# Performance work log

Hardware: AMD Instinct MI355X
Metric: run time of the kernel (lower is better)

Reference implementation:

```python
import jax, jax.numpy as jnp
import numpy as np

B, N, F, T, K, FO = 16, 1024, 64, 24, 3, 64


def setup_inputs() -> dict:
    key = jax.random.key(0)
    ks = jax.random.split(key, 8)
    sc = 0.05
    x = jax.random.normal(ks[0], (B, N, F, T), dtype=jnp.float32)
    W1 = jax.random.normal(ks[1], (T,), dtype=jnp.float32) * sc
    W2 = jax.random.normal(ks[2], (F, T), dtype=jnp.float32) * sc
    W3 = jax.random.normal(ks[3], (F,), dtype=jnp.float32) * sc
    bs = jax.random.normal(ks[4], (1, N, N), dtype=jnp.float32) * sc
    Vs = jax.random.normal(ks[5], (N, N), dtype=jnp.float32) * sc
    cheb = jax.random.normal(ks[6], (K, N, N), dtype=jnp.float32) * sc
    Theta = jax.random.normal(ks[7], (K, F, FO), dtype=jnp.float32) * sc
    return {"x": x, "W1": W1, "W2": W2, "W3": W3, "bs": bs, "Vs": Vs,
            "cheb": cheb, "Theta": Theta}


def spatial_attention(x, W1, W2, W3, bs, Vs):
    # x: (B,N,F,T) -> S: (B,N,N)
    lhs = jnp.einsum('bnft,t->bnf', x, W1)          # (B,N,F)
    lhs = jnp.einsum('bnf,ft->bnt', lhs, W2)        # (B,N,T)
    rhs = jnp.einsum('f,bnft->btn', W3, x)          # (B,T,N)
    product = jnp.einsum('bnt,btm->bnm', lhs, rhs)  # (B,N,N)
    S = jnp.einsum('ik,bkj->bij', Vs, jax.nn.sigmoid(product + bs))
    return jax.nn.softmax(S, axis=1)


def reference(x, W1, W2, W3, bs, Vs, cheb, Theta):
    # x: (B,N,F,T); cheb: (K,N,N); Theta: (K,F,FO)
    S = spatial_attention(x, W1, W2, W3, bs, Vs)    # (B,N,N)
    out = jnp.zeros((x.shape[0], x.shape[1], Theta.shape[2], x.shape[3]),
                    dtype=x.dtype)
    for k in range(cheb.shape[0]):                  # small fixed K
        Tat = cheb[k] * S                           # (B,N,N) attention-masked T_k
        # T_k_with_at.permute(0,2,1) @ graph_signal, vectorized over t
        r = jnp.einsum('bnm,bnft->bmft', Tat, x)    # (B,N,F,T)
        out = out + jnp.einsum('bmft,fo->bmot', r, Theta[k])
    return jax.nn.relu(out)                         # (B,N,FO,T)
```

## Files before the change

### kernel.cpp

```cpp
#include <hip/hip_runtime.h>
#include <math.h>

#define Bc 16
#define Nc 1024
#define Fc 64
#define Tc 24
#define Kc 3
#define FOc 64
#define Cc (Fc*Tc)
#define KKc (Kc*Nc)

typedef __attribute__((ext_vector_type(8))) short short8;
typedef __attribute__((ext_vector_type(8))) unsigned short u16x8;
typedef __attribute__((ext_vector_type(4))) float f32x4;

__device__ __forceinline__ unsigned short f2bf(float f) {
  unsigned u = __float_as_uint(f);
  u += 0x7fff + ((u >> 16) & 1);
  return (unsigned short)(u >> 16);
}
__device__ __forceinline__ float bf2f(unsigned short h) {
  return __uint_as_float((unsigned)h << 16);
}

#define GLL16(g, l) __builtin_amdgcn_global_load_lds( \
    (const __attribute__((address_space(1))) void*)(g), \
    (__attribute__((address_space(3))) void*)(l), 16, 0, 0)

__device__ __forceinline__ f32x4 mfma16(short8 a, short8 b, f32x4 c) {
  return __builtin_amdgcn_mfma_f32_16x16x32_bf16(a, b, c, 0, 0, 0);
}

__device__ __forceinline__ void gemm_core(
    const unsigned short* __restrict__ Ag, const unsigned short* __restrict__ Bg,
    int lda, int ldb, int K,
    unsigned short* As, unsigned short* Bs,
    int wave, int lane, f32x4 acc[4][4]) {
  int sr = lane >> 3;
  int sc = ((lane & 7) ^ sr) * 8;
  const unsigned short* a0 = Ag + (size_t)(wave * 32 + sr) * lda + sc;
  const unsigned short* b0 = Bg + (size_t)(wave * 32 + sr) * ldb + sc;
  unsigned short* asw = As + (wave * 32) * 64;
  unsigned short* bsw = Bs + (wave * 32) * 64;
  int rw = (wave >> 1) * 64, cw = (wave & 1) * 64;
  int frow = lane & 15;
  int q = lane >> 4;
  int p0 = (q ^ (frow & 7)) * 8;
  int p1 = ((q | 4) ^ (frow & 7)) * 8;
  for (int k0 = 0; k0 < K; k0 += 64) {
    #pragma unroll
    for (int c = 0; c < 4; ++c) {
      GLL16(a0 + (size_t)(c * 8) * lda + k0, asw + (c * 8) * 64);
      GLL16(b0 + (size_t)(c * 8) * ldb + k0, bsw + (c * 8) * 64);
    }
    __syncthreads();
    #pragma unroll
    for (int h = 0; h < 2; ++h) {
      int p = h ? p1 : p0;
      short8 afr[4], bfr[4];
      #pragma unroll
      for (int i = 0; i < 4; ++i)
        afr[i] = *(const short8*)&As[(rw + i * 16 + frow) * 64 + p];
      #pragma unroll
      for (int j = 0; j < 4; ++j)
        bfr[j] = *(const short8*)&Bs[(cw + j * 16 + frow) * 64 + p];
      #pragma unroll
      for (int i = 0; i < 4; ++i)
        #pragma unroll
        for (int j = 0; j < 4; ++j)
          acc[i][j] = mfma16(afr[i], bfr[j], acc[i][j]);
    }
    __syncthreads();
  }
}

__global__ __launch_bounds__(256) void xprep_kernel(
    const float* __restrict__ x, const float* __restrict__ W1,
    const float* __restrict__ W2, const float* __restrict__ W3,
    unsigned short* __restrict__ xt2, float* __restrict__ lhs,
    float* __restrict__ rhs) {
  __shared__ float ld[4 * 1560];
  __shared__ float af[4 * 64];
  int w = threadIdx.x >> 6, lane = threadIdx.x & 63;
  size_t n = (size_t)blockIdx.x * 4 + w;
  const float* xp = x + n * Cc;
  float* lw = ld + w * 1560;
  #pragma unroll
  for (int j = 0; j < 24; ++j) {
    int i = j * 64 + lane;
    int f = i / 24, t = i - f * 24;
    lw[t * 65 + f] = xp[i];
  }
  __syncthreads();
  float a = 0.f;
  #pragma unroll
  for (int t = 0; t < Tc; ++t) a += lw[t * 65 + lane] * W1[t];
  af[w * 64 + lane] = a;
  #pragma unroll
  for (int j = 0; j < 24; ++j)
    xt2[n * Cc + j * 64 + lane] = f2bf(lw[j * 65 + lane]);
  __syncthreads();
  if (lane < Tc) {
    float l = 0.f, r = 0.f;
    #pragma unroll 8
    for (int f = 0; f < Fc; ++f) {
      l += af[w * 64 + f] * W2[f * Tc + lane];
      r += W3[f] * lw[lane * 65 + f];
    }
    lhs[n * Tc + lane] = l;
    rhs[n * Tc + lane] = r;
  }
}

__global__ __launch_bounds__(256) void prodsigT_kernel(
    const float* __restrict__ lhs, const float* __restrict__ rhs,
    const float* __restrict__ bs, unsigned short* __restrict__ sigT) {
  int b = blockIdx.z;
  int p0 = blockIdx.y * 64, q0 = blockIdx.x * 64;
  __shared__ float Ls[64 * 25], Rs[64 * 25], Bt[64 * 65];
  int tid = threadIdx.x;
  const float* lp = lhs + ((size_t)b * Nc + q0) * Tc;
  const float* rp = rhs + ((size_t)b * Nc + p0) * Tc;
  for (int i = tid; i < 64 * Tc; i += 256) {
    Ls[(i / Tc) * 25 + i % Tc] = lp[i];
    Rs[(i / Tc) * 25 + i % Tc] = rp[i];
  }
  for (int i = tid; i < 1024; i += 256) {
    int qr = i >> 4, pc = (i & 15) * 4;
    *(float4*)&Bt[qr * 65 + pc] = *(const float4*)&bs[(size_t)(q0 + qr) * Nc + p0 + pc];
  }
  __syncthreads();
  int tx = tid % 16, ty = tid / 16;
  float acc[4][4] = {};
  for (int t = 0; t < Tc; ++t) {
    float rv[4], lv[4];
    #pragma unroll
    for (int i = 0; i < 4; ++i) rv[i] = Rs[(ty * 4 + i) * 25 + t];
    #pragma unroll
    for (int j = 0; j < 4; ++j) lv[j] = Ls[(tx * 4 + j) * 25 + t];
    #pragma unroll
    for (int i = 0; i < 4; ++i)
      #pragma unroll
      for (int j = 0; j < 4; ++j) acc[i][j] += rv[i] * lv[j];
  }
  #pragma unroll
  for (int i = 0; i < 4; ++i) {
    int p = p0 + ty * 4 + i;
    ushort4 o;
    float v0 = acc[i][0] + Bt[(tx * 4 + 0) * 65 + ty * 4 + i];
    float v1 = acc[i][1] + Bt[(tx * 4 + 1) * 65 + ty * 4 + i];
    float v2 = acc[i][2] + Bt[(tx * 4 + 2) * 65 + ty * 4 + i];
    float v3 = acc[i][3] + Bt[(tx * 4 + 3) * 65 + ty * 4 + i];
    o.x = f2bf(1.f / (1.f + __expf(-v0)));
    o.y = f2bf(1.f / (1.f + __expf(-v1)));
    o.z = f2bf(1.f / (1.f + __expf(-v2)));
    o.w = f2bf(1.f / (1.f + __expf(-v3)));
    *(ushort4*)&sigT[((size_t)b * Nc + p) * Nc + q0 + tx * 4] = o;
  }
}

__global__ __launch_bounds__(256) void cvt_vs_kernel(
    const float* __restrict__ Vs, unsigned short* __restrict__ Vsbf) {
  int i = (blockIdx.x * 256 + threadIdx.x) * 4;
  float4 v = *(const float4*)&Vs[i];
  ushort4 o;
  o.x = f2bf(v.x); o.y = f2bf(v.y); o.z = f2bf(v.z); o.w = f2bf(v.w);
  *(ushort4*)&Vsbf[i] = o;
}

__global__ __launch_bounds__(256) void chebT_kernel(
    const float* __restrict__ cheb, float* __restrict__ chebT) {
  int k = blockIdx.z;
  int n0 = blockIdx.y * 64, m0 = blockIdx.x * 64;
  __shared__ float t[64 * 65];
  const float* src = cheb + (size_t)k * Nc * Nc;
  float* dst = chebT + (size_t)k * Nc * Nc;
  int tid = threadIdx.x;
  #pragma unroll
  for (int s = 0; s < 4; ++s) {
    int nr = (tid >> 4) + s * 16, mc = (tid & 15) * 4;
    float4 v = *(const float4*)&src[(size_t)(n0 + nr) * Nc + m0 + mc];
    t[(mc + 0) * 65 + nr] = v.x;
    t[(mc + 1) * 65 + nr] = v.y;
    t[(mc + 2) * 65 + nr] = v.z;
    t[(mc + 3) * 65 + nr] = v.w;
  }
  __syncthreads();
  #pragma unroll
  for (int s = 0; s < 4; ++s) {
    int mr = (tid >> 4) + s * 16, nc = (tid & 15) * 4;
    float4 v = {t[mr * 65 + nc], t[mr * 65 + nc + 1], t[mr * 65 + nc + 2], t[mr * 65 + nc + 3]};
    *(float4*)&dst[(size_t)(m0 + mr) * Nc + n0 + nc] = v;
  }
}

__global__ __launch_bounds__(256) void tcat_kernel(
    const float* __restrict__ Theta, unsigned short* __restrict__ tcat) {
  int i = blockIdx.x * 256 + threadIdx.x;
  int m2 = i >> 6, f = i & 63;
  int k = m2 >> 6, o = m2 & 63;
  tcat[i] = (m2 < 192) ? f2bf(Theta[((size_t)k * Fc + f) * FOc + o])
                       : (unsigned short)0;
}

__global__ __launch_bounds__(256) void masksoft_kernel(
    const float* __restrict__ chebT, const unsigned short* __restrict__ ST,
    unsigned short* __restrict__ Acat, int bbase) {
  int m  = blockIdx.x & (Nc - 1);
  int bl = blockIdx.x >> 10;
  int tid = threadIdx.x;
  const unsigned short* sp = ST + ((size_t)(bbase + bl) * Nc + m) * Nc;
  ushort4 s4 = *(const ushort4*)(sp + tid * 4);
  float v0 = bf2f(s4.x), v1 = bf2f(s4.y), v2 = bf2f(s4.z), v3 = bf2f(s4.w);
  __shared__ float redm[4], reds[4];
  int wave = tid >> 6, lane = tid & 63;
  float mx = fmaxf(fmaxf(v0, v1), fmaxf(v2, v3));
  #pragma unroll
  for (int off = 32; off; off >>= 1) mx = fmaxf(mx, __shfl_xor(mx, off));
  if (lane == 0) redm[wave] = mx;
  __syncthreads();
  mx = fmaxf(fmaxf(redm[0], redm[1]), fmaxf(redm[2], redm[3]));
  float e0 = __expf(v0 - mx), e1 = __expf(v1 - mx);
  float e2 = __expf(v2 - mx), e3 = __expf(v3 - mx);
  float sm = e0 + e1 + e2 + e3;
  #pragma unroll
  for (int off = 32; off; off >>= 1) sm += __shfl_xor(sm, off);
  if (lane == 0) reds[wave] = sm;
  __syncthreads();
  float inv = 1.f / (reds[0] + reds[1] + reds[2] + reds[3]);
  e0 *= inv; e1 *= inv; e2 *= inv; e3 *= inv;
  unsigned short* ap = Acat + ((size_t)bl * Nc + m) * KKc + tid * 4;
  #pragma unroll
  for (int k = 0; k < Kc; ++k) {
    float4 c = *(const float4*)&chebT[((size_t)k * Nc + m) * Nc + tid * 4];
    ushort4 o;
    o.x = f2bf(c.x * e0); o.y = f2bf(c.y * e1);
    o.z = f2bf(c.z * e2); o.w = f2bf(c.w * e3);
    *(ushort4*)(ap + k * Nc) = o;
  }
}

template <int MODE>
__global__ __launch_bounds__(256) void mfma_gemm_bt(
    const unsigned short* __restrict__ A, const unsigned short* __restrict__ B,
    void* __restrict__ Cv, int K, int CN,
    long long Abatch, long long Bbatch, long long Cbatch) {
  __shared__ unsigned short As[128 * 64];
  __shared__ unsigned short Bs[128 * 64];
  int b = blockIdx.z;
  int tid = threadIdx.x, wave = tid >> 6, lane = tid & 63;
  const unsigned short* Ag = A + (size_t)b * Abatch + (size_t)blockIdx.y * 128 * K;
  const unsigned short* Bg = B + (size_t)b * Bbatch + (size_t)blockIdx.x * 128 * K;
  f32x4 zero = {0.f, 0.f, 0.f, 0.f};
  f32x4 acc[4][4];
  #pragma unroll
  for (int i = 0; i < 4; ++i)
    #pragma unroll
    for (int j = 0; j < 4; ++j) acc[i][j] = zero;
  gemm_core(Ag, Bg, K, K, K, As, Bs, wave, lane, acc);
  int rw = (wave >> 1) * 64, cw = (wave & 1) * 64;
  int q = lane >> 4, cl = lane & 15;
  if (MODE == 0) {
    unsigned short* Cg = (unsigned short*)Cv + (size_t)b * Cbatch
                         + (size_t)blockIdx.y * 128 * CN + (size_t)blockIdx.x * 128;
    #pragma unroll
    for (int i = 0; i < 4; ++i)
      #pragma unroll
      for (int j = 0; j < 4; ++j)
        #pragma unroll
        for (int e = 0; e < 4; ++e)
          Cg[(size_t)(rw + i * 16 + q * 4 + e) * CN + cw + j * 16 + cl] =
              f2bf(acc[i][j][e]);
  } else {
    float* Cg = (float*)Cv + (size_t)b * Cbatch
                + (size_t)blockIdx.y * 128 * CN + (size_t)blockIdx.x * 128;
    #pragma unroll
    for (int i = 0; i < 4; ++i)
      #pragma unroll
      for (int j = 0; j < 4; ++j)
        #pragma unroll
        for (int e = 0; e < 4; ++e)
          Cg[(size_t)(rw + i * 16 + q * 4 + e) * CN + cw + j * 16 + cl] =
              fmaxf(acc[i][j][e], 0.f);
  }
}

__global__ __launch_bounds__(256) void y2_gemm(
    const unsigned short* __restrict__ tcat, const unsigned short* __restrict__ xt2,
    unsigned short* __restrict__ ycat, int bbase) {
  __shared__ unsigned short As[128 * 64];
  __shared__ unsigned short Bs[128 * 64];
  int z = blockIdx.z;
  int bl = z / 24, t = z - bl * 24;
  int tid = threadIdx.x, wave = tid >> 6, lane = tid & 63;
  const unsigned short* Ag = tcat + (size_t)blockIdx.y * 128 * 64;
  const unsigned short* Bg = xt2 + ((size_t)(bbase + bl) * Nc + (size_t)blockIdx.x * 128) * Cc
                             + (size_t)t * 64;
  f32x4 zero = {0.f, 0.f, 0.f, 0.f};
  f32x4 acc[4][4];
  #pragma unroll
  for (int i = 0; i < 4; ++i)
    #pragma unroll
    for (int j = 0; j < 4; ++j) acc[i][j] = zero;
  gemm_core(Ag, Bg, 64, Cc, 64, As, Bs, wave, lane, acc);
  int rw = (wave >> 1) * 64, cw = (wave & 1) * 64;
  int q = lane >> 4, cl = lane & 15;
  unsigned short* yb = ycat + (size_t)bl * Cc * KKc + (size_t)t * KKc;
  #pragma unroll
  for (int i = 0; i < 4; ++i)
    #pragma unroll
    for (int e = 0; e < 4; ++e) {
      int m2 = blockIdx.y * 128 + rw + i * 16 + q * 4 + e;
      if (m2 < 192) {
        int kk = m2 >> 6, o = m2 & 63;
        unsigned short* dst = yb + (size_t)o * 24 * KKc + kk * Nc;
        #pragma unroll
        for (int j = 0; j < 4; ++j)
          dst[blockIdx.x * 128 + cw + j * 16 + cl] = f2bf(acc[i][j][e]);
      }
    }
}

extern "C" void kernel_launch(void* const* d_in, const int* in_sizes, int n_in,
                              void* d_out, int out_size, void* d_ws, size_t ws_size,
                              hipStream_t stream) {
  const float* x     = (const float*)d_in[0];
  const float* W1    = (const float*)d_in[1];
  const float* W2    = (const float*)d_in[2];
  const float* W3    = (const float*)d_in[3];
  const float* bs    = (const float*)d_in[4];
  const float* Vs    = (const float*)d_in[5];
  const float* cheb  = (const float*)d_in[6];
  const float* Theta = (const float*)d_in[7];
  float* out = (float*)d_out;

  char* w = (char*)d_ws;
  unsigned short* ycat = (unsigned short*)w;
  float* lhs = (float*)w;
  float* rhs = (float*)(w + 1572864);
  unsigned short* sigT = (unsigned short*)(w + 3145728);
  unsigned short* Vsbf = (unsigned short*)(w + 36700160);
  unsigned short* Acat = (unsigned short*)(w + 75497472);
  unsigned short* ST   = (unsigned short*)(w + 125829120);
  float* chebT         = (float*)(w + 159383552);
  unsigned short* xt2  = (unsigned short*)(w + 171966464);
  unsigned short* tcat = (unsigned short*)(w + 222298112);

  xprep_kernel<<<Bc * Nc / 4, 256, 0, stream>>>(x, W1, W2, W3, xt2, lhs, rhs);
  prodsigT_kernel<<<dim3(Nc / 64, Nc / 64, Bc), 256, 0, stream>>>(lhs, rhs, bs, sigT);
  cvt_vs_kernel<<<Nc * Nc / 1024, 256, 0, stream>>>(Vs, Vsbf);
  mfma_gemm_bt<0><<<dim3(Nc / 128, Nc / 128, Bc), 256, 0, stream>>>(
      sigT, Vsbf, ST, Nc, Nc, (long long)Nc * Nc, 0LL, (long long)Nc * Nc);
  chebT_kernel<<<dim3(Nc / 64, Nc / 64, Kc), 256, 0, stream>>>(cheb, chebT);
  tcat_kernel<<<64, 256, 0, stream>>>(Theta, tcat);

  for (int half = 0; half < 2; ++half) {
    int bbase = half * 8;
    masksoft_kernel<<<8 * Nc, 256, 0, stream>>>(chebT, ST, Acat, bbase);
    y2_gemm<<<dim3(Nc / 128, 2, 8 * 24), 256, 0, stream>>>(tcat, xt2, ycat, bbase);
    mfma_gemm_bt<1><<<dim3(Cc / 128, Nc / 128, 8), 256, 0, stream>>>(
        Acat, ycat, out + (size_t)bbase * Nc * Cc, KKc, Cc,
        (long long)Nc * KKc, (long long)Cc * KKc, (long long)Nc * Cc);
  }
}
```

Measured before the change: 566.5 us.

## Compute attention product with bf16 MFMA GEMM, merge small prep kernels, single pass

The scalar FP32 prodsigT kernel is replaced by an MFMA GEMM mode that takes bf16 lhs/rhs zero-padded to K=64 and fuses the bias add and sigmoid into its epilogue, reading a pre-transposed bias. The Vs conversion, Theta packing and bias transpose are merged into one misc kernel to cut launches. If the workspace is large enough, the batch is processed in one pass instead of two halves, avoiding extra launches. The product operands now lose precision to bf16, and the bias-transposed layout must line up with the GEMM's output indexing.

```diff
diff --git a/kernel.cpp b/kernel.cpp
--- a/kernel.cpp
+++ b/kernel.cpp
@@ -77,8 +77,8 @@
 __global__ __launch_bounds__(256) void xprep_kernel(
     const float* __restrict__ x, const float* __restrict__ W1,
     const float* __restrict__ W2, const float* __restrict__ W3,
-    unsigned short* __restrict__ xt2, float* __restrict__ lhs,
-    float* __restrict__ rhs) {
+    unsigned short* __restrict__ xt2, unsigned short* __restrict__ lhsb,
+    unsigned short* __restrict__ rhsb) {
   __shared__ float ld[4 * 1560];
   __shared__ float af[4 * 64];
   int w = threadIdx.x >> 6, lane = threadIdx.x & 63;
@@ -100,72 +100,57 @@
   for (int j = 0; j < 24; ++j)
     xt2[n * Cc + j * 64 + lane] = f2bf(lw[j * 65 + lane]);
   __syncthreads();
+  float l = 0.f, r = 0.f;
   if (lane < Tc) {
-    float l = 0.f, r = 0.f;
     #pragma unroll 8
     for (int f = 0; f < Fc; ++f) {
       l += af[w * 64 + f] * W2[f * Tc + lane];
       r += W3[f] * lw[lane * 65 + f];
     }
-    lhs[n * Tc + lane] = l;
-    rhs[n * Tc + lane] = r;
-  }
-}
-
-__global__ __launch_bounds__(256) void prodsigT_kernel(
-    const float* __restrict__ lhs, const float* __restrict__ rhs,
-    const float* __restrict__ bs, unsigned short* __restrict__ sigT) {
-  int b = blockIdx.z;
-  int p0 = blockIdx.y * 64, q0 = blockIdx.x * 64;
-  __shared__ float Ls[64 * 25], Rs[64 * 25], Bt[64 * 65];
-  int tid = threadIdx.x;
-  const float* lp = lhs + ((size_t)b * Nc + q0) * Tc;
-  const float* rp = rhs + ((size_t)b * Nc + p0) * Tc;
-  for (int i = tid; i < 64 * Tc; i += 256) {
-    Ls[(i / Tc) * 25 + i % Tc] = lp[i];
-    Rs[(i / Tc) * 25 + i % Tc] = rp[i];
-  }
-  for (int i = tid; i < 1024; i += 256) {
-    int qr = i >> 4, pc = (i & 15) * 4;
-    *(float4*)&Bt[qr * 65 + pc] = *(const float4*)&bs[(size_t)(q0 + qr) * Nc + p0 + pc];
-  }
-  __syncthreads();
-  int tx = tid % 16, ty = tid / 16;
-  float acc[4][4] = {};
-  for (int t = 0; t < Tc; ++t) {
-    float rv[4], lv[4];
-    #pragma unroll
-    for (int i = 0; i < 4; ++i) rv[i] = Rs[(ty * 4 + i) * 25 + t];
-    #pragma unroll
-    for (int j = 0; j < 4; ++j) lv[j] = Ls[(tx * 4 + j) * 25 + t];
-    #pragma unroll
-    for (int i = 0; i < 4; ++i)
-      #pragma unroll
-      for (int j = 0; j < 4; ++j) acc[i][j] += rv[i] * lv[j];
-  }
-  #pragma unroll
-  for (int i = 0; i < 4; ++i) {
-    int p = p0 + ty * 4 + i;
+  }
+  lhsb[n * 64 + lane] = (lane < Tc) ? f2bf(l) : (unsigned short)0;
+  rhsb[n * 64 + lane] = (lane < Tc) ? f2bf(r) : (unsigned short)0;
+}
+
+__global__ __launch_bounds__(256) void misc_kernel(
+    const float* __restrict__ Vs, const float* __restrict__ Theta,
+    const float* __restrict__ bs, unsigned short* __restrict__ Vsbf,
+    unsigned short* __restrict__ tcat, float* __restrict__ bsT) {
+  __shared__ float t[64 * 65];
+  int bid = blockIdx.x, tid = threadIdx.x;
+  if (bid < 1024) {
+    int i = (bid * 256 + tid) * 4;
+    float4 v = *(const float4*)&Vs[i];
     ushort4 o;
-    float v0 = acc[i][0] + Bt[(tx * 4 + 0) * 65 + ty * 4 + i];
-    float v1 = acc[i][1] + Bt[(tx * 4 + 1) * 65 + ty * 4 + i];
-    float v2 = acc[i][2] + Bt[(tx * 4 + 2) * 65 + ty * 4 + i];
-    float v3 = acc[i][3] + Bt[(tx * 4 + 3) * 65 + ty * 4 + i];
-    o.x = f2bf(1.f / (1.f + __expf(-v0)));
-    o.y = f2bf(1.f / (1.f + __expf(-v1)));
-    o.z = f2bf(1.f / (1.f + __expf(-v2)));
-    o.w = f2bf(1.f / (1.f + __expf(-v3)));
-    *(ushort4*)&sigT[((size_t)b * Nc + p) * Nc + q0 + tx * 4] = o;
-  }
-}
-
-__global__ __launch_bounds__(256) void cvt_vs_kernel(
-    const float* __restrict__ Vs, unsigned short* __restrict__ Vsbf) {
-  int i = (blockIdx.x * 256 + threadIdx.x) * 4;
-  float4 v = *(const float4*)&Vs[i];
-  ushort4 o;
-  o.x = f2bf(v.x); o.y = f2bf(v.y); o.z = f2bf(v.z); o.w = f2bf(v.w);
-  *(ushort4*)&Vsbf[i] = o;
+    o.x = f2bf(v.x); o.y = f2bf(v.y); o.z = f2bf(v.z); o.w = f2bf(v.w);
+    *(ushort4*)&Vsbf[i] = o;
+  } else if (bid < 1088) {
+    int i = (bid - 1024) * 256 + tid;
+    int m2 = i >> 6, f = i & 63;
+    int k = m2 >> 6, o = m2 & 63;
+    tcat[i] = (m2 < 192) ? f2bf(Theta[((size_t)k * Fc + f) * FOc + o])
+                         : (unsigned short)0;
+  } else {
+    int id = bid - 1088;
+    int p0 = (id >> 4) * 64, q0 = (id & 15) * 64;
+    #pragma unroll
+    for (int s = 0; s < 4; ++s) {
+      int qr = (tid >> 4) + s * 16, pc = (tid & 15) * 4;
+      float4 v = *(const float4*)&bs[(size_t)(q0 + qr) * Nc + p0 + pc];
+      t[(pc + 0) * 65 + qr] = v.x;
+      t[(pc + 1) * 65 + qr] = v.y;
+      t[(pc + 2) * 65 + qr] = v.z;
+      t[(pc + 3) * 65 + qr] = v.w;
+    }
+    __syncthreads();
+    #pragma unroll
+    for (int s = 0; s < 4; ++s) {
+      int pr = (tid >> 4) + s * 16, qc = (tid & 15) * 4;
+      float4 v = {t[pr * 65 + qc], t[pr * 65 + qc + 1],
+                  t[pr * 65 + qc + 2], t[pr * 65 + qc + 3]};
+      *(float4*)&bsT[(size_t)(p0 + pr) * Nc + q0 + qc] = v;
+    }
+  }
 }
 
 __global__ __launch_bounds__(256) void chebT_kernel(
@@ -192,15 +177,6 @@
     float4 v = {t[mr * 65 + nc], t[mr * 65 + nc + 1], t[mr * 65 + nc + 2], t[mr * 65 + nc + 3]};
     *(float4*)&dst[(size_t)(m0 + mr) * Nc + n0 + nc] = v;
   }
-}
-
-__global__ __launch_bounds__(256) void tcat_kernel(
-    const float* __restrict__ Theta, unsigned short* __restrict__ tcat) {
-  int i = blockIdx.x * 256 + threadIdx.x;
-  int m2 = i >> 6, f = i & 63;
-  int k = m2 >> 6, o = m2 & 63;
-  tcat[i] = (m2 < 192) ? f2bf(Theta[((size_t)k * Fc + f) * FOc + o])
-                       : (unsigned short)0;
 }
 
 __global__ __launch_bounds__(256) void masksoft_kernel(
@@ -243,7 +219,7 @@
 template <int MODE>
 __global__ __launch_bounds__(256) void mfma_gemm_bt(
     const unsigned short* __restrict__ A, const unsigned short* __restrict__ B,
-    void* __restrict__ Cv, int K, int CN,
+    void* __restrict__ Cv, const float* __restrict__ bias, int K, int CN,
     long long Abatch, long long Bbatch, long long Cbatch) {
   __shared__ unsigned short As[128 * 64];
   __shared__ unsigned short Bs[128 * 64];
@@ -260,29 +236,25 @@
   gemm_core(Ag, Bg, K, K, K, As, Bs, wave, lane, acc);
   int rw = (wave >> 1) * 64, cw = (wave & 1) * 64;
   int q = lane >> 4, cl = lane & 15;
-  if (MODE == 0) {
-    unsigned short* Cg = (unsigned short*)Cv + (size_t)b * Cbatch
-                         + (size_t)blockIdx.y * 128 * CN + (size_t)blockIdx.x * 128;
-    #pragma unroll
-    for (int i = 0; i < 4; ++i)
+  #pragma unroll
+  for (int i = 0; i < 4; ++i)
+    #pragma unroll
+    for (int e = 0; e < 4; ++e) {
+      size_t P = (size_t)blockIdx.y * 128 + rw + i * 16 + q * 4 + e;
       #pragma unroll
-      for (int j = 0; j < 4; ++j)
-        #pragma unroll
-        for (int e = 0; e < 4; ++e)
-          Cg[(size_t)(rw + i * 16 + q * 4 + e) * CN + cw + j * 16 + cl] =
-              f2bf(acc[i][j][e]);
-  } else {
-    float* Cg = (float*)Cv + (size_t)b * Cbatch
-                + (size_t)blockIdx.y * 128 * CN + (size_t)blockIdx.x * 128;
-    #pragma unroll
-    for (int i = 0; i < 4; ++i)
-      #pragma unroll
-      for (int j = 0; j < 4; ++j)
-        #pragma unroll
-        for (int e = 0; e < 4; ++e)
-          Cg[(size_t)(rw + i * 16 + q * 4 + e) * CN + cw + j * 16 + cl] =
-              fmaxf(acc[i][j][e], 0.f);
-  }
+      for (int j = 0; j < 4; ++j) {
+        size_t Q = (size_t)blockIdx.x * 128 + cw + j * 16 + cl;
+        if (MODE == 0) {
+          ((unsigned short*)Cv)[(size_t)b * Cbatch + P * CN + Q] = f2bf(acc[i][j][e]);
+        } else if (MODE == 1) {
+          ((float*)Cv)[(size_t)b * Cbatch + P * CN + Q] = fmaxf(acc[i][j][e], 0.f);
+        } else {
+          float v = acc[i][j][e] + bias[P * CN + Q];
+          ((unsigned short*)Cv)[(size_t)b * Cbatch + P * CN + Q] =
+              f2bf(1.f / (1.f + __expf(-v)));
+        }
+      }
+    }
 }
 
 __global__ __launch_bounds__(256) void y2_gemm(
@@ -334,32 +306,41 @@
   const float* Theta = (const float*)d_in[7];
   float* out = (float*)d_out;
 
+  int passes, blcount;
+  if (ws_size >= 348160000ULL) { passes = 1; blcount = 16; }
+  else                         { passes = 2; blcount = 8;  }
+
   char* w = (char*)d_ws;
+  size_t Y  = (size_t)blcount * Cc * KKc * 2;
+  size_t A2 = (size_t)blcount * Nc * KKc * 2;
   unsigned short* ycat = (unsigned short*)w;
-  float* lhs = (float*)w;
-  float* rhs = (float*)(w + 1572864);
-  unsigned short* sigT = (unsigned short*)(w + 3145728);
-  unsigned short* Vsbf = (unsigned short*)(w + 36700160);
-  unsigned short* Acat = (unsigned short*)(w + 75497472);
-  unsigned short* ST   = (unsigned short*)(w + 125829120);
-  float* chebT         = (float*)(w + 159383552);
-  unsigned short* xt2  = (unsigned short*)(w + 171966464);
-  unsigned short* tcat = (unsigned short*)(w + 222298112);
-
-  xprep_kernel<<<Bc * Nc / 4, 256, 0, stream>>>(x, W1, W2, W3, xt2, lhs, rhs);
-  prodsigT_kernel<<<dim3(Nc / 64, Nc / 64, Bc), 256, 0, stream>>>(lhs, rhs, bs, sigT);
-  cvt_vs_kernel<<<Nc * Nc / 1024, 256, 0, stream>>>(Vs, Vsbf);
-  mfma_gemm_bt<0><<<dim3(Nc / 128, Nc / 128, Bc), 256, 0, stream>>>(
-      sigT, Vsbf, ST, Nc, Nc, (long long)Nc * Nc, 0LL, (long long)Nc * Nc);
-  chebT_kernel<<<dim3(Nc / 64, Nc / 64, Kc), 256, 0, stream>>>(cheb, chebT);
-  tcat_kernel<<<64, 256, 0, stream>>>(Theta, tcat);
-
-  for (int half = 0; half < 2; ++half) {
-    int bbase = half * 8;
-    masksoft_kernel<<<8 * Nc, 256, 0, stream>>>(chebT, ST, Acat, bbase);
-    y2_gemm<<<dim3(Nc / 128, 2, 8 * 24), 256, 0, stream>>>(tcat, xt2, ycat, bbase);
-    mfma_gemm_bt<1><<<dim3(Cc / 128, Nc / 128, 8), 256, 0, stream>>>(
-        Acat, ycat, out + (size_t)bbase * Nc * Cc, KKc, Cc,
+  unsigned short* Acat = (unsigned short*)(w + Y);
+  unsigned short* ST   = (unsigned short*)(w + Y + A2);
+  float* chebT         = (float*)(w + Y + A2 + 33554432);
+  unsigned short* xt2  = (unsigned short*)(w + Y + A2 + 46137344);
+  unsigned short* tcat = (unsigned short*)(w + Y + A2 + 96468992);
+  unsigned short* lhsb = (unsigned short*)w;
+  unsigned short* rhsb = (unsigned short*)(w + 2097152);
+  unsigned short* sigT = (unsigned short*)(w + 4194304);
+  float* bsT           = (float*)(w + 37748736);
+  unsigned short* Vsbf = (unsigned short*)(w + 41943040);
+
+  xprep_kernel<<<Bc * Nc / 4, 256, 0, stream>>>(x, W1, W2, W3, xt2, lhsb, rhsb);
+  misc_kernel<<<1344, 256, 0, stream>>>(Vs, Theta, bs, Vsbf, tcat, bsT);
+  mfma_gemm_bt<2><<<dim3(8, 8, 16), 256, 0, stream>>>(
+      rhsb, lhsb, sigT, bsT, 64, Nc,
+      (long long)Nc * 64, (long long)Nc * 64, (long long)Nc * Nc);
+  mfma_gemm_bt<0><<<dim3(8, 8, 16), 256, 0, stream>>>(
+      sigT, Vsbf, ST, nullptr, Nc, Nc,
+      (long long)Nc * Nc, 0LL, (long long)Nc * Nc);
+  chebT_kernel<<<dim3(16, 16, 3), 256, 0, stream>>>(cheb, chebT);
+
+  for (int pass = 0; pass < passes; ++pass) {
+    int bbase = pass * blcount;
+    masksoft_kernel<<<blcount * Nc, 256, 0, stream>>>(chebT, ST, Acat, bbase);
+    y2_gemm<<<dim3(Nc / 128, 2, blcount * 24), 256, 0, stream>>>(tcat, xt2, ycat, bbase);
+    mfma_gemm_bt<1><<<dim3(Cc / 128, Nc / 128, blcount), 256, 0, stream>>>(
+        Acat, ycat, out + (size_t)bbase * Nc * Cc, nullptr, KKc, Cc,
         (long long)Nc * KKc, (long long)Cc * KKc, (long long)Nc * Cc);
   }
 }
```

New measurement: 557.1 us. Within noise of the previous version (-1.7%).
